# Optimization experiments

Measured on AMD Instinct MI355X. Metric: run time of the kernel, lower is better.

Reference implementation:

```python
import jax, jax.numpy as jnp
import numpy as np

COST_CLASS, COST_BBOX, COST_GIOU = 1.0, 5.0, 2.0


def _lsa(cost):
    """Rectangular linear sum assignment (minimize), Jonker-Volgenant style.
    Returns (row_ind, col_ind) like scipy.optimize.linear_sum_assignment."""
    c = np.asarray(cost, dtype=np.float64)
    transposed = c.shape[0] > c.shape[1]
    if transposed:
        c = c.T
    n, m = c.shape  # n <= m
    INF = 1e18
    u = np.zeros(n + 1)
    v = np.zeros(m + 1)
    p = np.zeros(m + 1, dtype=np.int64)   # p[j]: row (1-based) matched to col j, 0 = free
    way = np.zeros(m + 1, dtype=np.int64)
    for i in range(1, n + 1):
        p[0] = i
        j0 = 0
        minv = np.full(m + 1, INF)
        used = np.zeros(m + 1, dtype=bool)
        while True:
            used[j0] = True
            i0 = p[j0]
            cur = c[i0 - 1, :] - u[i0] - v[1:]
            mv = minv[1:]
            upd = (~used[1:]) & (cur < mv)
            mv[upd] = cur[upd]
            way[1:][upd] = j0
            masked = np.where(used[1:], INF, mv)
            j1 = int(np.argmin(masked)) + 1
            delta = masked[j1 - 1]
            u[p[used]] += delta
            v[used] -= delta
            minv[1:][~used[1:]] -= delta
            j0 = j1
            if p[j0] == 0:
                break
        while j0:
            j1 = way[j0]
            p[j0] = p[j1]
            j0 = j1
    rows = p[1:] - 1
    cols = np.arange(m)
    keep = rows >= 0
    ri, ci = rows[keep], cols[keep]
    if transposed:
        ri, ci = ci, ri
    order = np.argsort(ri)
    return ri[order], ci[order]


def _solve_blocks(cost, n_per):
    """cost: np [Q, B*n_per]; solve LSA per diagonal block, return 0/1 solution."""
    Q, T = cost.shape
    B = T // n_per
    sol = np.zeros((Q, T), dtype=np.float32)
    for b in range(B):
        ri, ci = _lsa(cost[:, b * n_per:(b + 1) * n_per])
        sol[ri, b * n_per + ci] = 1.0
    return sol


def box_cxcywh_to_xyxy(b):
    cx, cy, w, h = jnp.split(b, 4, axis=-1)
    return jnp.concatenate([cx - 0.5 * w, cy - 0.5 * h, cx + 0.5 * w, cy + 0.5 * h], axis=-1)


def generalized_box_iou(b1, b2):
    # b1: [N,4] xyxy, b2: [M,4] xyxy -> [N,M]
    area1 = (b1[:, 2] - b1[:, 0]) * (b1[:, 3] - b1[:, 1])
    area2 = (b2[:, 2] - b2[:, 0]) * (b2[:, 3] - b2[:, 1])
    lt = jnp.maximum(b1[:, None, :2], b2[None, :, :2])
    rb = jnp.minimum(b1[:, None, 2:], b2[None, :, 2:])
    wh = jnp.clip(rb - lt, 0.0)
    inter = wh[..., 0] * wh[..., 1]
    union = area1[:, None] + area2[None, :] - inter
    iou = inter / union
    ltc = jnp.minimum(b1[:, None, :2], b2[None, :, :2])
    rbc = jnp.maximum(b1[:, None, 2:], b2[None, :, 2:])
    whc = jnp.clip(rbc - ltc, 0.0)
    areac = whc[..., 0] * whc[..., 1]
    return iou - (areac - union) / areac


def build_cost(pred_logits, pred_boxes, tgt_labels, tgt_boxes, n_per):
    B, Q, C = pred_logits.shape
    out_prob = jax.nn.softmax(pred_logits.reshape(B * Q, C), axis=-1)
    out_bbox = pred_boxes.reshape(B * Q, 4)
    cost_class = -out_prob[:, tgt_labels]                                  # [N,T]
    cost_bbox = jnp.sum(jnp.abs(out_bbox[:, None, :] - tgt_boxes[None, :, :]), axis=-1)  # L1 cdist
    cost_giou = -generalized_box_iou(box_cxcywh_to_xyxy(out_bbox), box_cxcywh_to_xyxy(tgt_boxes))
    cm = COST_BBOX * cost_bbox + COST_CLASS * cost_class + COST_GIOU * cost_giou
    cm = cm.reshape(B, Q, B, n_per)
    blocks = cm[jnp.arange(B), :, jnp.arange(B), :]        # diagonal blocks [B,Q,n_per]
    return jnp.transpose(blocks, (1, 0, 2)).reshape(Q, B * n_per)  # hstack -> [Q, T]


def setup_inputs() -> dict:
    key = jax.random.key(0)
    k1, k2, k3, k4 = jax.random.split(key, 4)
    B, Q, C, n_per = 16, 900, 92, 32
    T = B * n_per
    return {
        "pred_logits": jax.random.normal(k1, (B, Q, C), dtype=jnp.float32),
        "pred_boxes": jax.random.uniform(k2, (B, Q, 4), dtype=jnp.float32),
        "tgt_labels": jax.random.randint(k3, (T,), 0, C, dtype=jnp.int64),
        "tgt_boxes": jax.random.uniform(k4, (T, 4), dtype=jnp.float32),
        "n_targets": n_per,
    }


def reference(pred_logits, pred_boxes, tgt_labels, tgt_boxes, n_targets):
    n_per = int(n_targets)
    cost = build_cost(pred_logits, pred_boxes, tgt_labels, tgt_boxes, n_per)
    sol = jax.pure_callback(
        lambda c: _solve_blocks(np.asarray(c, dtype=np.float64), n_per),
        jax.ShapeDtypeStruct(cost.shape, jnp.float32),
        cost,
    )
    return sol
```

## Files before the change

kernel.cpp:

```cpp
#include <hip/hip_runtime.h>
#include <math.h>

#define BB 16
#define QQ 900
#define CC 92
#define NP 32
#define TT (BB*NP)
#define RSTRIDE 1024
#define NT 512

__device__ __forceinline__ double mkdbl(int lo, int hi) {
    return __longlong_as_double(((long long)hi << 32) | (unsigned int)lo);
}
__device__ __forceinline__ double readlane_dbl(double x, int s) {
    long long l = __double_as_longlong(x);
    int lo = __builtin_amdgcn_readlane((int)l, s);
    int hi = __builtin_amdgcn_readlane((int)(l >> 32), s);
    return mkdbl(lo, hi);
}

#define DPP_MIN64(CTRL)                                                       \
    {                                                                         \
        long long _l = __double_as_longlong(m);                               \
        int _lo = (int)_l, _hi = (int)(_l >> 32);                             \
        int _olo = __builtin_amdgcn_update_dpp(_lo, _lo, CTRL, 0xf, 0xf, false); \
        int _ohi = __builtin_amdgcn_update_dpp(_hi, _hi, CTRL, 0xf, 0xf, false); \
        m = fmin(m, mkdbl(_olo, _ohi));                                       \
    }

#define OFF_COST 0
#define SZ_COST  (NP * RSTRIDE * 4)
#define OFF_U    (OFF_COST + SZ_COST)
#define OFF_V    (OFF_U + 264)
#define OFF_P    (OFF_V + 7208)
#define OFF_MAX  (OFF_P + 3604)
#define OFF_SUM  (OFF_MAX + 3600)
#define OFF_FLAG (OFF_SUM + 3600)
#define DYN_BYTES (OFF_FLAG + 128)

__launch_bounds__(NT)
__global__ void matcher_kernel(const float* __restrict__ logits,
                               const float* __restrict__ pboxes,
                               const int*   __restrict__ labels,
                               const float* __restrict__ tboxes,
                               float* __restrict__ out)
{
    extern __shared__ char smem[];
    float*  s_cost = (float*)(smem + OFF_COST);
    double* s_u    = (double*)(smem + OFF_U);
    double* s_v    = (double*)(smem + OFF_V);
    int*    s_p    = (int*)(smem + OFF_P);
    float*  s_max  = (float*)(smem + OFF_MAX);
    float*  s_sum  = (float*)(smem + OFF_SUM);
    volatile int* s_flag = (volatile int*)(smem + OFF_FLAG);

    const int b    = blockIdx.x;
    const int tid  = threadIdx.x;
    const int wv   = tid >> 6;
    const int lane = tid & 63;

    const float* lg = logits + (size_t)b * QQ * CC;
    if (tid < 32) s_flag[tid] = 0;
    for (int q = tid; q < QQ; q += NT) {
        const float4* row4 = (const float4*)(lg + q * CC);
        float mx = -INFINITY;
        #pragma unroll
        for (int k = 0; k < 23; ++k) {
            float4 x = row4[k];
            mx = fmaxf(mx, x.x); mx = fmaxf(mx, x.y);
            mx = fmaxf(mx, x.z); mx = fmaxf(mx, x.w);
        }
        float s = 0.f;
        #pragma unroll
        for (int k = 0; k < 23; ++k) {
            float4 x = row4[k];
            s += expf(x.x - mx); s += expf(x.y - mx);
            s += expf(x.z - mx); s += expf(x.w - mx);
        }
        s_max[q] = mx;
        s_sum[q] = s;
    }
    __syncthreads();

    const float* pb = pboxes + (size_t)b * QQ * 4;
    const float* tb = tboxes + (size_t)b * NP * 4;
    const int*   lb = labels + b * NP;

    if (wv != 0) {
        for (int t = wv - 1; t < NP; t += 7) {
            const float t0 = tb[t*4+0], t1 = tb[t*4+1],
                        t2 = tb[t*4+2], t3 = tb[t*4+3];
            const int   lt = lb[t];
            const float tx1 = t0 - 0.5f*t2, ty1 = t1 - 0.5f*t3;
            const float tx2 = t0 + 0.5f*t2, ty2 = t1 + 0.5f*t3;
            const float area2 = (tx2-tx1)*(ty2-ty1);
            #pragma unroll 4
            for (int it = 0; it < 16; ++it) {
                int q = (it << 6) + lane;
                float val = 0.f;
                if (q < QQ) {
                    float l    = lg[q * CC + lt];
                    float prob = expf(l - s_max[q]) / s_sum[q];
                    float cclass = -prob;
                    float p0 = pb[q*4+0], p1 = pb[q*4+1],
                          p2 = pb[q*4+2], p3 = pb[q*4+3];
                    float cbbox = fabsf(p0-t0) + fabsf(p1-t1)
                                + fabsf(p2-t2) + fabsf(p3-t3);
                    float px1 = p0 - 0.5f*p2, py1 = p1 - 0.5f*p3;
                    float px2 = p0 + 0.5f*p2, py2 = p1 + 0.5f*p3;
                    float area1 = (px2-px1)*(py2-py1);
                    float ltx = fmaxf(px1,tx1), lty = fmaxf(py1,ty1);
                    float rbx = fminf(px2,tx2), rby = fminf(py2,ty2);
                    float wx = fmaxf(rbx-ltx, 0.f), wy = fmaxf(rby-lty, 0.f);
                    float inter = wx*wy;
                    float uni = area1 + area2 - inter;
                    float iou = inter / uni;
                    float cx1 = fminf(px1,tx1), cy1 = fminf(py1,ty1);
                    float cx2 = fmaxf(px2,tx2), cy2 = fmaxf(py2,ty2);
                    float cwx = fmaxf(cx2-cx1, 0.f), cwy = fmaxf(cy2-cy1, 0.f);
                    float areac = cwx*cwy;
                    float giou = iou - (areac - uni) / areac;
                    val = 5.f*cbbox + 1.f*cclass + 2.f*(-giou);
                }
                s_cost[t * RSTRIDE + q] = val;
            }
            asm volatile("s_waitcnt lgkmcnt(0)" ::: "memory");
            if (lane == 0) s_flag[t] = 1;
        }
    } else {
        for (int j = lane; j <= QQ; j += 64) { s_p[j] = 0; s_v[j] = 0.0; }
        if (lane <= NP) s_u[lane] = 0.0;
        asm volatile("s_waitcnt lgkmcnt(0)" ::: "memory");

        int acol = 0;
        const float4* cbase4 = (const float4*)s_cost;

        double vreg[16];
        #pragma unroll
        for (int k = 0; k < 16; ++k) vreg[k] = 0.0;

        unsigned used0 = 0;
        #pragma unroll
        for (int k = 0; k < 16; ++k) {
            int col = 4 * lane + ((k >> 2) << 8) + (k & 3) + 1;
            if (col > QQ) used0 |= 1u << k;
        }

        int nv = 0;
        for (int i = 1; i <= NP; ++i) {
            while (nv < i) {
                if (s_flag[nv]) ++nv;
                else __builtin_amdgcn_s_sleep(2);
            }

            unsigned used = used0;

            int i0 = i, j1prev = 0, T = 0;
            int path_reg = 1, row_reg = 1;

            float4 cf[4];
            {
                const float4* crow4 = cbase4 + (size_t)(i0 - 1) * (RSTRIDE / 4);
                #pragma unroll
                for (int k = 0; k < 4; ++k) cf[k] = crow4[lane + (k << 6)];
            }

            for (int t = 1;; ++t) {
                if (lane == t) row_reg = i0;
                if (j1prev) {
                    int qp = j1prev - 1;
                    if (((qp >> 2) & 63) == lane)
                        used |= 1u << (((qp >> 8) << 2) | (qp & 3));
                }

                double key[16];
                #pragma unroll
                for (int k = 0; k < 4; ++k) {
                    const float* cp = (const float*)&cf[k];
                    #pragma unroll
                    for (int e2 = 0; e2 < 4; ++e2) {
                        int kk  = 4 * k + e2;
                        int col = 4 * lane + (k << 8) + e2 + 1;
                        double d = (double)cp[e2] - vreg[kk];
                        long long bits =
                            (__double_as_longlong(d) & ~2047LL) | (long long)col;
                        key[kk] = ((used >> kk) & 1u)
                                      ? 1e300 : __longlong_as_double(bits);
                    }
                }
                double a0 = fmin(key[0], key[1]),   a1 = fmin(key[2], key[3]);
                double a2 = fmin(key[4], key[5]),   a3 = fmin(key[6], key[7]);
                double a4 = fmin(key[8], key[9]),   a5 = fmin(key[10], key[11]);
                double a6 = fmin(key[12], key[13]), a7 = fmin(key[14], key[15]);
                double b0 = fmin(a0, a1), b1 = fmin(a2, a3);
                double b2 = fmin(a4, a5), b3 = fmin(a6, a7);
                double m  = fmin(fmin(b0, b1), fmin(b2, b3));

                DPP_MIN64(0x111);
                DPP_MIN64(0x112);
                DPP_MIN64(0x114);
                DPP_MIN64(0x118);
                DPP_MIN64(0x142);
                DPP_MIN64(0x143);

                int wlo = __builtin_amdgcn_readlane((int)__double_as_longlong(m), 63);
                int j1  = wlo & 2047;

                if (lane == t) path_reg = j1;

                unsigned long long mask = __ballot(acol == j1);
                if (mask == 0) { T = t; break; }
                int L = (int)__builtin_ctzll(mask);
                i0 = L + 1;
                j1prev = j1;

                const float4* crow4 = cbase4 + (size_t)L * (RSTRIDE / 4);
                #pragma unroll
                for (int k = 0; k < 4; ++k) cf[k] = crow4[lane + (k << 6)];
            }

            const int  rt  = row_reg;
            const int  myj = path_reg;
            const bool act = (lane >= 1 && lane <= T);
            double mydelta = 0.0, uu = 0.0, vv = 0.0;
            if (act) {
                double cD = (double)s_cost[(rt - 1) * RSTRIDE + (myj - 1)];
                mydelta = (cD - s_u[rt]) - s_v[myj];
                uu = s_u[rt];
                vv = s_v[myj];
            }
            for (int s = 1; s <= T; ++s) {
                double ds = readlane_dbl(mydelta, s);
                int    js = __builtin_amdgcn_readlane(path_reg, s);
                int    rs = __builtin_amdgcn_readlane(row_reg, s);
                if (lane >= 1 && lane <= s) uu += ds;
                if (lane >= 1 && lane <  s) vv -= ds;
                if (rs == lane + 1) acol = js;
            }
            if (act) {
                s_u[rt]  = uu;
                s_v[myj] = vv;
                s_p[myj] = rt;
            }
            for (int s = 1; s <= T; ++s) {
                int    js  = __builtin_amdgcn_readlane(path_reg, s);
                double vvs = readlane_dbl(vv, s);
                #pragma unroll
                for (int k = 0; k < 16; ++k) {
                    int col = 4 * lane + ((k >> 2) << 8) + (k & 3) + 1;
                    if (col == js) vreg[k] = vvs;
                }
            }
        }
    }
    __syncthreads();

    for (int e = tid; e < QQ * 8; e += NT) {
        int q = e >> 3;
        int f = e & 7;
        int pq = s_p[q + 1];
        int base = 4 * f;
        float4 o;
        o.x = (pq == base + 1) ? 1.f : 0.f;
        o.y = (pq == base + 2) ? 1.f : 0.f;
        o.z = (pq == base + 3) ? 1.f : 0.f;
        o.w = (pq == base + 4) ? 1.f : 0.f;
        ((float4*)(out + (size_t)q * TT + b * NP))[f] = o;
    }
}

extern "C" void kernel_launch(void* const* d_in, const int* in_sizes, int n_in,
                              void* d_out, int out_size, void* d_ws, size_t ws_size,
                              hipStream_t stream) {
    const float* logits = (const float*)d_in[0];
    const float* pboxes = (const float*)d_in[1];
    const int*   labels = (const int*)  d_in[2];
    const float* tboxes = (const float*)d_in[3];
    float* out = (float*)d_out;

    (void)hipFuncSetAttribute((const void*)matcher_kernel,
                              hipFuncAttributeMaxDynamicSharedMemorySize,
                              DYN_BYTES);

    matcher_kernel<<<BB, NT, DYN_BYTES, stream>>>(logits, pboxes, labels,
                                                  tboxes, out);
}
```

Measured before the change: 120.2 us.

## Split matcher into denom, cost, walk and epilogue kernels via workspace

Splits the single 16-block fused kernel into four launches when a workspace is provided. Softmax denominators and the cost matrix are computed across many blocks in global memory. A walk kernel then loads the cost rows into shared memory through producer waves and runs the serial assignment, and a separate wide kernel writes the one-hot output. This spreads the cost build and output write over the whole GPU instead of 16 CUs. In exchange it adds launch overhead and a global-memory round trip for the cost matrix.

After: 116.9 us. -2.8%, faster.

```diff
diff --git a/kernel.cpp b/kernel.cpp
--- a/kernel.cpp
+++ b/kernel.cpp
@@ -9,6 +9,12 @@
 #define RSTRIDE 1024
 #define NT 512
 
+#define WSC_COST 0
+#define WSC_MAX  (BB*NP*RSTRIDE*4)
+#define WSC_SUM  (WSC_MAX + BB*QQ*4)
+#define WSC_A    (WSC_SUM + BB*QQ*4)
+#define WS_NEED  (WSC_A + TT*4)
+
 __device__ __forceinline__ double mkdbl(int lo, int hi) {
     return __longlong_as_double(((long long)hi << 32) | (unsigned int)lo);
 }
@@ -27,6 +33,276 @@
         int _ohi = __builtin_amdgcn_update_dpp(_hi, _hi, CTRL, 0xf, 0xf, false); \
         m = fmin(m, mkdbl(_olo, _ohi));                                       \
     }
+
+__launch_bounds__(256)
+__global__ void denom_kernel(const float* __restrict__ logits,
+                             float* __restrict__ wmax,
+                             float* __restrict__ wsum)
+{
+    int idx = blockIdx.x * 256 + threadIdx.x;
+    if (idx >= BB * QQ) return;
+    const float4* row4 = (const float4*)(logits + (size_t)idx * CC);
+    float mx = -INFINITY;
+    #pragma unroll
+    for (int k = 0; k < 23; ++k) {
+        float4 x = row4[k];
+        mx = fmaxf(mx, x.x); mx = fmaxf(mx, x.y);
+        mx = fmaxf(mx, x.z); mx = fmaxf(mx, x.w);
+    }
+    float s = 0.f;
+    #pragma unroll
+    for (int k = 0; k < 23; ++k) {
+        float4 x = row4[k];
+        s += expf(x.x - mx); s += expf(x.y - mx);
+        s += expf(x.z - mx); s += expf(x.w - mx);
+    }
+    wmax[idx] = mx;
+    wsum[idx] = s;
+}
+
+__launch_bounds__(256)
+__global__ void cost_kernel(const float* __restrict__ logits,
+                            const float* __restrict__ pboxes,
+                            const int*   __restrict__ labels,
+                            const float* __restrict__ tboxes,
+                            const float* __restrict__ wmax,
+                            const float* __restrict__ wsum,
+                            float* __restrict__ wcost)
+{
+    const int r = blockIdx.x;
+    const int b = r >> 5, t = r & 31;
+    const float* lg = logits + (size_t)b * QQ * CC;
+    const float* pb = pboxes + (size_t)b * QQ * 4;
+    const float* tb = tboxes + (size_t)b * NP * 4;
+    const float* smax = wmax + b * QQ;
+    const float* ssum = wsum + b * QQ;
+
+    const float t0 = tb[t*4+0], t1 = tb[t*4+1], t2 = tb[t*4+2], t3 = tb[t*4+3];
+    const int   lt = labels[b * NP + t];
+    const float tx1 = t0 - 0.5f*t2, ty1 = t1 - 0.5f*t3;
+    const float tx2 = t0 + 0.5f*t2, ty2 = t1 + 0.5f*t3;
+    const float area2 = (tx2-tx1)*(ty2-ty1);
+
+    float* crow = wcost + (size_t)r * RSTRIDE;
+    for (int q = threadIdx.x; q < RSTRIDE; q += 256) {
+        float val = 0.f;
+        if (q < QQ) {
+            float l    = lg[q * CC + lt];
+            float prob = expf(l - smax[q]) / ssum[q];
+            float cclass = -prob;
+            float p0 = pb[q*4+0], p1 = pb[q*4+1], p2 = pb[q*4+2], p3 = pb[q*4+3];
+            float cbbox = fabsf(p0-t0) + fabsf(p1-t1)
+                        + fabsf(p2-t2) + fabsf(p3-t3);
+            float px1 = p0 - 0.5f*p2, py1 = p1 - 0.5f*p3;
+            float px2 = p0 + 0.5f*p2, py2 = p1 + 0.5f*p3;
+            float area1 = (px2-px1)*(py2-py1);
+            float ltx = fmaxf(px1,tx1), lty = fmaxf(py1,ty1);
+            float rbx = fminf(px2,tx2), rby = fminf(py2,ty2);
+            float wx = fmaxf(rbx-ltx, 0.f), wy = fmaxf(rby-lty, 0.f);
+            float inter = wx*wy;
+            float uni = area1 + area2 - inter;
+            float iou = inter / uni;
+            float cx1 = fminf(px1,tx1), cy1 = fminf(py1,ty1);
+            float cx2 = fmaxf(px2,tx2), cy2 = fmaxf(py2,ty2);
+            float cwx = fmaxf(cx2-cx1, 0.f), cwy = fmaxf(cy2-cy1, 0.f);
+            float areac = cwx*cwy;
+            float giou = iou - (areac - uni) / areac;
+            val = 5.f*cbbox + 1.f*cclass + 2.f*(-giou);
+        }
+        crow[q] = val;
+    }
+}
+
+#define C_OFF_COST 0
+#define C_SZ_COST  (NP * RSTRIDE * 4)
+#define C_OFF_U    (C_OFF_COST + C_SZ_COST)
+#define C_OFF_V    (C_OFF_U + 264)
+#define C_OFF_FLAG (C_OFF_V + 7208)
+#define C_DYN      (C_OFF_FLAG + 128)
+
+__launch_bounds__(256)
+__global__ void walk_kernel(const float* __restrict__ wcost,
+                            int* __restrict__ wa)
+{
+    extern __shared__ char smem[];
+    float*  s_cost = (float*)(smem + C_OFF_COST);
+    double* s_u    = (double*)(smem + C_OFF_U);
+    double* s_v    = (double*)(smem + C_OFF_V);
+    volatile int* s_flag = (volatile int*)(smem + C_OFF_FLAG);
+
+    const int b    = blockIdx.x;
+    const int tid  = threadIdx.x;
+    const int wv   = tid >> 6;
+    const int lane = tid & 63;
+
+    if (tid < 32) s_flag[tid] = 0;
+    __syncthreads();
+
+    if (wv != 0) {
+        for (int t = wv - 1; t < NP; t += 3) {
+            const float4* src =
+                (const float4*)(wcost + ((size_t)(b * NP + t) * RSTRIDE));
+            float4* dst = (float4*)(s_cost + t * RSTRIDE);
+            float4 v0 = src[lane];
+            float4 v1 = src[lane + 64];
+            float4 v2 = src[lane + 128];
+            float4 v3 = src[lane + 192];
+            dst[lane]       = v0;
+            dst[lane + 64]  = v1;
+            dst[lane + 128] = v2;
+            dst[lane + 192] = v3;
+            asm volatile("s_waitcnt vmcnt(0) lgkmcnt(0)" ::: "memory");
+            if (lane == 0) s_flag[t] = 1;
+        }
+        return;
+    }
+
+    for (int j = lane; j <= QQ; j += 64) s_v[j] = 0.0;
+    if (lane <= NP) s_u[lane] = 0.0;
+    asm volatile("s_waitcnt lgkmcnt(0)" ::: "memory");
+
+    int acol = 0;
+    const float4* cbase4 = (const float4*)s_cost;
+
+    double vreg[16];
+    #pragma unroll
+    for (int k = 0; k < 16; ++k) vreg[k] = 0.0;
+
+    unsigned used0 = 0;
+    #pragma unroll
+    for (int k = 0; k < 16; ++k) {
+        int col = 4 * lane + ((k >> 2) << 8) + (k & 3) + 1;
+        if (col > QQ) used0 |= 1u << k;
+    }
+
+    int nv = 0;
+    for (int i = 1; i <= NP; ++i) {
+        while (nv < i) {
+            if (s_flag[nv]) ++nv;
+            else __builtin_amdgcn_s_sleep(2);
+        }
+
+        unsigned used = used0;
+
+        int i0 = i, j1prev = 0, T = 0;
+        int path_reg = 1, row_reg = 1;
+
+        float4 cf[4];
+        {
+            const float4* crow4 = cbase4 + (size_t)(i0 - 1) * (RSTRIDE / 4);
+            #pragma unroll
+            for (int k = 0; k < 4; ++k) cf[k] = crow4[lane + (k << 6)];
+        }
+
+        for (int t = 1;; ++t) {
+            if (lane == t) row_reg = i0;
+            if (j1prev) {
+                int qp = j1prev - 1;
+                if (((qp >> 2) & 63) == lane)
+                    used |= 1u << (((qp >> 8) << 2) | (qp & 3));
+            }
+
+            double key[16];
+            #pragma unroll
+            for (int k = 0; k < 4; ++k) {
+                const float* cp = (const float*)&cf[k];
+                #pragma unroll
+                for (int e2 = 0; e2 < 4; ++e2) {
+                    int kk  = 4 * k + e2;
+                    int col = 4 * lane + (k << 8) + e2 + 1;
+                    double d = (double)cp[e2] - vreg[kk];
+                    long long bits =
+                        (__double_as_longlong(d) & ~2047LL) | (long long)col;
+                    key[kk] = ((used >> kk) & 1u)
+                                  ? 1e300 : __longlong_as_double(bits);
+                }
+            }
+            double a0 = fmin(key[0], key[1]),   a1 = fmin(key[2], key[3]);
+            double a2 = fmin(key[4], key[5]),   a3 = fmin(key[6], key[7]);
+            double a4 = fmin(key[8], key[9]),   a5 = fmin(key[10], key[11]);
+            double a6 = fmin(key[12], key[13]), a7 = fmin(key[14], key[15]);
+            double b0 = fmin(a0, a1), b1 = fmin(a2, a3);
+            double b2 = fmin(a4, a5), b3 = fmin(a6, a7);
+            double m  = fmin(fmin(b0, b1), fmin(b2, b3));
+
+            DPP_MIN64(0x111);
+            DPP_MIN64(0x112);
+            DPP_MIN64(0x114);
+            DPP_MIN64(0x118);
+            DPP_MIN64(0x142);
+            DPP_MIN64(0x143);
+
+            int wlo = __builtin_amdgcn_readlane((int)__double_as_longlong(m), 63);
+            int j1  = wlo & 2047;
+
+            if (lane == t) path_reg = j1;
+
+            unsigned long long mask = __ballot(acol == j1);
+            if (mask == 0) { T = t; break; }
+            int L = (int)__builtin_ctzll(mask);
+            i0 = L + 1;
+            j1prev = j1;
+
+            const float4* crow4 = cbase4 + (size_t)L * (RSTRIDE / 4);
+            #pragma unroll
+            for (int k = 0; k < 4; ++k) cf[k] = crow4[lane + (k << 6)];
+        }
+
+        const int  rt  = row_reg;
+        const int  myj = path_reg;
+        const bool act = (lane >= 1 && lane <= T);
+        double mydelta = 0.0, uu = 0.0, vv = 0.0;
+        if (act) {
+            double cD = (double)s_cost[(rt - 1) * RSTRIDE + (myj - 1)];
+            mydelta = (cD - s_u[rt]) - s_v[myj];
+            uu = s_u[rt];
+            vv = s_v[myj];
+        }
+        for (int s = 1; s <= T; ++s) {
+            double ds = readlane_dbl(mydelta, s);
+            int    js = __builtin_amdgcn_readlane(path_reg, s);
+            int    rs = __builtin_amdgcn_readlane(row_reg, s);
+            if (lane >= 1 && lane <= s) uu += ds;
+            if (lane >= 1 && lane <  s) vv -= ds;
+            if (rs == lane + 1) acol = js;
+        }
+        if (act) {
+            s_u[rt]  = uu;
+            s_v[myj] = vv;
+        }
+        for (int s = 1; s <= T; ++s) {
+            int    js  = __builtin_amdgcn_readlane(path_reg, s);
+            double vvs = readlane_dbl(vv, s);
+            #pragma unroll
+            for (int k = 0; k < 16; ++k) {
+                int col = 4 * lane + ((k >> 2) << 8) + (k & 3) + 1;
+                if (col == js) vreg[k] = vvs;
+            }
+        }
+    }
+
+    if (lane < NP) wa[b * NP + lane] = acol - 1;
+}
+
+__launch_bounds__(256)
+__global__ void epilogue_kernel(const int* __restrict__ wa,
+                                float* __restrict__ out)
+{
+    int idx = blockIdx.x * 256 + threadIdx.x;
+    if (idx >= QQ * BB * 8) return;
+    int q   = idx >> 7;
+    int rem = idx & 127;
+    int b   = rem >> 3, f = rem & 7;
+    int base = b * NP + 4 * f;
+    int a0 = wa[base + 0], a1 = wa[base + 1];
+    int a2 = wa[base + 2], a3 = wa[base + 3];
+    float4 o;
+    o.x = (a0 == q) ? 1.f : 0.f;
+    o.y = (a1 == q) ? 1.f : 0.f;
+    o.z = (a2 == q) ? 1.f : 0.f;
+    o.w = (a3 == q) ? 1.f : 0.f;
+    ((float4*)(out + (size_t)q * TT + b * NP))[f] = o;
+}
 
 #define OFF_COST 0
 #define SZ_COST  (NP * RSTRIDE * 4)
@@ -152,19 +428,15 @@
                 if (s_flag[nv]) ++nv;
                 else __builtin_amdgcn_s_sleep(2);
             }
-
             unsigned used = used0;
-
             int i0 = i, j1prev = 0, T = 0;
             int path_reg = 1, row_reg = 1;
-
             float4 cf[4];
             {
                 const float4* crow4 = cbase4 + (size_t)(i0 - 1) * (RSTRIDE / 4);
                 #pragma unroll
                 for (int k = 0; k < 4; ++k) cf[k] = crow4[lane + (k << 6)];
             }
-
             for (int t = 1;; ++t) {
                 if (lane == t) row_reg = i0;
                 if (j1prev) {
@@ -172,7 +444,6 @@
                     if (((qp >> 2) & 63) == lane)
                         used |= 1u << (((qp >> 8) << 2) | (qp & 3));
                 }
-
                 double key[16];
                 #pragma unroll
                 for (int k = 0; k < 4; ++k) {
@@ -195,30 +466,20 @@
                 double b0 = fmin(a0, a1), b1 = fmin(a2, a3);
                 double b2 = fmin(a4, a5), b3 = fmin(a6, a7);
                 double m  = fmin(fmin(b0, b1), fmin(b2, b3));
-
-                DPP_MIN64(0x111);
-                DPP_MIN64(0x112);
-                DPP_MIN64(0x114);
-                DPP_MIN64(0x118);
-                DPP_MIN64(0x142);
-                DPP_MIN64(0x143);
-
+                DPP_MIN64(0x111); DPP_MIN64(0x112); DPP_MIN64(0x114);
+                DPP_MIN64(0x118); DPP_MIN64(0x142); DPP_MIN64(0x143);
                 int wlo = __builtin_amdgcn_readlane((int)__double_as_longlong(m), 63);
                 int j1  = wlo & 2047;
-
                 if (lane == t) path_reg = j1;
-
                 unsigned long long mask = __ballot(acol == j1);
                 if (mask == 0) { T = t; break; }
                 int L = (int)__builtin_ctzll(mask);
                 i0 = L + 1;
                 j1prev = j1;
-
                 const float4* crow4 = cbase4 + (size_t)L * (RSTRIDE / 4);
                 #pragma unroll
                 for (int k = 0; k < 4; ++k) cf[k] = crow4[lane + (k << 6)];
             }
-
             const int  rt  = row_reg;
             const int  myj = path_reg;
             const bool act = (lane >= 1 && lane <= T);
@@ -278,10 +539,26 @@
     const float* tboxes = (const float*)d_in[3];
     float* out = (float*)d_out;
 
-    (void)hipFuncSetAttribute((const void*)matcher_kernel,
-                              hipFuncAttributeMaxDynamicSharedMemorySize,
-                              DYN_BYTES);
-
-    matcher_kernel<<<BB, NT, DYN_BYTES, stream>>>(logits, pboxes, labels,
-                                                  tboxes, out);
-}
+    if (d_ws != nullptr && ws_size >= (size_t)WS_NEED) {
+        float* wcost = (float*)((char*)d_ws + WSC_COST);
+        float* wmax  = (float*)((char*)d_ws + WSC_MAX);
+        float* wsum  = (float*)((char*)d_ws + WSC_SUM);
+        int*   wa    = (int*)  ((char*)d_ws + WSC_A);
+
+        (void)hipFuncSetAttribute((const void*)walk_kernel,
+                                  hipFuncAttributeMaxDynamicSharedMemorySize,
+                                  C_DYN);
+
+        denom_kernel<<<(BB*QQ + 255)/256, 256, 0, stream>>>(logits, wmax, wsum);
+        cost_kernel<<<BB*NP, 256, 0, stream>>>(logits, pboxes, labels, tboxes,
+                                               wmax, wsum, wcost);
+        walk_kernel<<<BB, 256, C_DYN, stream>>>(wcost, wa);
+        epilogue_kernel<<<(QQ*BB*8 + 255)/256, 256, 0, stream>>>(wa, out);
+    } else {
+        (void)hipFuncSetAttribute((const void*)matcher_kernel,
+                                  hipFuncAttributeMaxDynamicSharedMemorySize,
+                                  DYN_BYTES);
+        matcher_kernel<<<BB, NT, DYN_BYTES, stream>>>(logits, pboxes, labels,
+                                                      tboxes, out);
+    }
+}
```
